# Kernel optimization log

Measured on AMD Instinct MI355X. Metric: run time of the kernel, lower is better.

The kernel has to match this reference:

```python
import jax, jax.numpy as jnp
import numpy as np

B, C, L = 1024, 256, 16   # nodes, channels (num_features), num_ell (dim of 0e+1o+2e+3o)
E = 10                    # num_elements
K3, K2, K1 = 23, 4, 1     # U-matrix path counts for correlation orders 3,2,1


def setup_inputs() -> dict:
    key = jax.random.key(0)
    ks = jax.random.split(key, 8)
    return {
        "x": jax.random.normal(ks[0], (B, C, L), jnp.float32),
        "y": jax.random.normal(ks[1], (B, E), jnp.float32),
        # U buffers (generalized Clebsch-Gordan, here random stand-ins of the right shapes)
        "U3": jax.random.normal(ks[2], (L, L, L, K3), jnp.float32),
        "U2": jax.random.normal(ks[3], (L, L, K2), jnp.float32),
        "U1": jax.random.normal(ks[4], (L, K1), jnp.float32),
        # per-element weights, scaled by 1/num_params as in the module
        "W3": jax.random.normal(ks[5], (E, K3, C), jnp.float32) / K3,
        "W2": jax.random.normal(ks[6], (E, K2, C), jnp.float32) / K2,
        "W1": jax.random.normal(ks[7], (E, K1, C), jnp.float32) / K1,
    }


def reference(x, y, U3, U2, U1, W3, W2, W1):
    # symmetric_cp, irrep_out lmax=0 (scalar output), correlation=3.
    # Main (nu=3): out[b,c,w,v] = sum_{i,k,e} U3[w,v,i,k] W3[e,k,c] x[b,c,i] y[b,e]
    # Efficient order: element-select weights, outer-product over (i,k), then one GEMM with U3.
    w3 = jnp.einsum('ekc,be->bkc', W3, y)              # [B,K3,C]
    q = jnp.einsum('bkc,bci->bcik', w3, x)             # [B,C,L,K3]
    out = jnp.einsum('wvik,bcik->bcwv', U3, q)         # [B,C,L,L]
    # nu=2: weighting then feature contraction
    w2 = jnp.einsum('ekc,be->bkc', W2, y)              # [B,K2,C]
    c2 = jnp.einsum('wvk,bkc->bcwv', U2, w2) + out     # [B,C,L,L]
    out = jnp.einsum('bcwi,bci->bcw', c2, x)           # [B,C,L]
    # nu=1
    w1 = jnp.einsum('ekc,be->bkc', W1, y)              # [B,K1,C]
    c1 = jnp.einsum('wk,bkc->bcw', U1, w1) + out       # [B,C,L]
    out = jnp.einsum('bci,bci->bc', c1, x)             # [B,C]
    return out.reshape(out.shape[0], -1)
```

## Files before the change

kernel.cpp:

```cpp
#include <hip/hip_runtime.h>


#define B_   1024
#define C_   256
#define L_   16
#define E_   10
#define K3_  23
#define K2_  4

#define NM3  816
#define NM2  136
#define MTOT 992
#define NCH2 61
#define STSTR 68

using f32x4   = __attribute__((ext_vector_type(4))) float;
using f32x16  = __attribute__((ext_vector_type(16))) float;
using short8v = __attribute__((ext_vector_type(8))) short;

__device__ __host__ __forceinline__ constexpr int tri_(int n) { return n * (n + 1) / 2; }
__device__ __host__ __forceinline__ constexpr int tet_(int n) { return n * (n + 1) * (n + 2) / 6; }

struct MTab { unsigned char a[MTOT], b[MTOT], c[MTOT]; };
constexpr MTab mkMT() {
  MTab t = {};
  int m = 0;
  for (int a = 0; a < 16; a++)
    for (int b = a; b < 16; b++)
      for (int c = b; c < 16; c++) { t.a[m] = a; t.b[m] = b; t.c[m] = c; ++m; }
  for (int a = 0; a < 16; a++)
    for (int b = a; b < 16; b++) { t.a[m] = a; t.b[m] = b; t.c[m] = 16; ++m; }
  for (int a = 0; a < 16; a++) { t.a[m] = a; t.b[m] = 16; t.c[m] = 16; ++m; }
  while (m < MTOT) { t.a[m] = 17; t.b[m] = 17; t.c[m] = 17; ++m; }
  return t;
}
constexpr MTab MT = mkMT();

__global__ void prep_kernel(const float* __restrict__ U3, const float* __restrict__ U2,
                            const float* __restrict__ U1, unsigned short* __restrict__ wsFrag) {
  __shared__ float sRow[16][36];
  const int ch = blockIdx.x;
  const int tid = threadIdx.x;
  if (tid < 16) {
    const int m = ch * 16 + tid;
    for (int i = 0; i < 36; i++) sRow[tid][i] = 0.f;
    if (m < NM3) {
      int ia = 0;
      while (tet_(16) - tet_(16 - (ia + 1)) <= m) ia++;
      int rem = m - (tet_(16) - tet_(16 - ia));
      int ib = ia;
      while (tri_(16 - ia) - tri_(16 - (ib + 1)) <= rem) ib++;
      int ic = ib + (rem - (tri_(16 - ia) - tri_(16 - ib)));
      int pw[6] = {ia, ia, ib, ib, ic, ic};
      int pv[6] = {ib, ic, ia, ic, ia, ib};
      int pi[6] = {ic, ib, ic, ia, ib, ia};
      bool use[6];
      for (int p = 0; p < 6; p++) {
        bool dup = false;
        for (int q = 0; q < p; q++)
          dup = dup || (pw[p] == pw[q] && pv[p] == pv[q] && pi[p] == pi[q]);
        use[p] = !dup;
      }
      for (int k = 0; k < K3_; k++) {
        float s = 0.f;
        for (int p = 0; p < 6; p++)
          if (use[p]) s += U3[((pw[p] * L_ + pv[p]) * L_ + pi[p]) * K3_ + k];
        sRow[tid][k] = s;
      }
    } else if (m < NM3 + NM2) {
      const int pidx = m - NM3;
      int ia = 0;
      while (136 - tri_(16 - (ia + 1)) <= pidx) ia++;
      int ib = ia + (pidx - (136 - tri_(16 - ia)));
      for (int k2 = 0; k2 < K2_; k2++) {
        float s = U2[(ia * L_ + ib) * K2_ + k2];
        if (ia != ib) s += U2[(ib * L_ + ia) * K2_ + k2];
        sRow[tid][23 + k2] = s;
      }
    } else if (m < NM3 + NM2 + L_) {
      sRow[tid][27] = U1[m - NM3 - NM2];
    }
  }
  __syncthreads();
  {
    const int lane = tid;
    unsigned short v16[8];
    for (int j = 0; j < 8; j++) {
      float v = sRow[(lane >> 5) * 8 + j][lane & 31];
      unsigned vb = __float_as_uint(v) + 0x8000u;
      v16[j] = (unsigned short)(vb >> 16);
    }
    unsigned* dst = (unsigned*)(wsFrag + ((size_t)ch * 64 + lane) * 8);
    for (int p = 0; p < 4; p++)
      dst[p] = (unsigned)v16[2 * p] | ((unsigned)v16[2 * p + 1] << 16);
  }
}

__device__ __forceinline__ void lane32_swap(unsigned& a, unsigned& b) {
#if defined(__has_builtin) && __has_builtin(__builtin_amdgcn_permlane32_swap)
  auto r = __builtin_amdgcn_permlane32_swap((int)a, (int)b, false, false);
  a = (unsigned)r[0];
  b = (unsigned)r[1];
#else
  asm volatile("v_permlane32_swap_b32 %0, %1" : "+v"(a), "+v"(b));
#endif
}

template <int M>
__device__ __forceinline__ float pval(const float (&XX)[16]) {
  if constexpr (MT.a[M] == 17) return 0.f;
  else if constexpr (MT.b[M] == 16) return XX[MT.a[M]];
  else if constexpr (MT.c[M] == 16) return XX[MT.a[M]] * XX[MT.b[M]];
  else return XX[MT.a[M]] * XX[MT.b[M]] * XX[MT.c[M]];
}

template <int CH, int I>
__device__ __forceinline__ void pk_pair(const float (&XX)[16],
                                        unsigned& o0, unsigned& o1) {
  {
    float p0 = pval<CH * 16 + 2 * I>(XX);
    float p1 = pval<CH * 16 + 2 * I + 1>(XX);
    asm("v_cvt_pk_bf16_f32 %0, %1, %2" : "=v"(o0) : "v"(p0), "v"(p1));
  }
  {
    float p0 = pval<CH * 16 + 8 + 2 * I>(XX);
    float p1 = pval<CH * 16 + 8 + 2 * I + 1>(XX);
    asm("v_cvt_pk_bf16_f32 %0, %1, %2" : "=v"(o1) : "v"(p0), "v"(p1));
  }
  lane32_swap(o0, o1);
}

template <int CH>
__device__ __forceinline__ void chunk_body(
    const float (&XX)[16], const float4* __restrict__ Bg, int lane,
    float4& nb0, float4& nb1, f32x16& acc0, f32x16& acc1) {
  unsigned pk0[4], pk1[4];
  pk_pair<CH, 0>(XX, pk0[0], pk1[0]);
  pk_pair<CH, 1>(XX, pk0[1], pk1[1]);
  pk_pair<CH, 2>(XX, pk0[2], pk1[2]);
  pk_pair<CH, 3>(XX, pk0[3], pk1[3]);

  float4 bh;
  if constexpr ((CH & 1) == 0) bh = nb0; else bh = nb1;
  if constexpr (CH + 2 < NCH2) {
    if constexpr ((CH & 1) == 0) nb0 = Bg[(CH + 2) * 64 + lane];
    else                         nb1 = Bg[(CH + 2) * 64 + lane];
  }
  short8v A0, A1, BH;
  __builtin_memcpy(&A0, pk0, 16);
  __builtin_memcpy(&A1, pk1, 16);
  __builtin_memcpy(&BH, &bh, 16);

  acc0 = __builtin_amdgcn_mfma_f32_32x32x16_bf16(A0, BH, acc0, 0, 0, 0);
  acc1 = __builtin_amdgcn_mfma_f32_32x32x16_bf16(A1, BH, acc1, 0, 0, 0);
}

template <int CH>
struct Loop {
  static __device__ __forceinline__ void run(
      const float (&XX)[16], const float4* __restrict__ Bg, int lane,
      float4& nb0, float4& nb1, f32x16& acc0, f32x16& acc1) {
    chunk_body<CH>(XX, Bg, lane, nb0, nb1, acc0, acc1);
    Loop<CH + 1>::run(XX, Bg, lane, nb0, nb1, acc0, acc1);
  }
};
template <>
struct Loop<NCH2> {
  static __device__ __forceinline__ void run(
      const float (&)[16], const float4* __restrict__, int,
      float4&, float4&, f32x16&, f32x16&) {}
};

__global__ __launch_bounds__(64, 2) void symcon_kernel(
    const float* __restrict__ x,
    const float* __restrict__ y,
    const float* __restrict__ W3,
    const float* __restrict__ W2,
    const float* __restrict__ W1,
    const unsigned short* __restrict__ wsFrag,
    float* __restrict__ out)
{
  __shared__ __attribute__((aligned(16))) float sT[28 * STSTR];

  const int lane = threadIdx.x;
  const int bb = blockIdx.x;
  const int b = bb >> 2;
  const int c = (bb & 3) * 64 + lane;

  float XX[16];
  {
    const float4* xg = (const float4*)(x + ((size_t)b * C_ + c) * L_);
    #pragma unroll
    for (int i = 0; i < 4; i++) {
      float4 v = xg[i];
      XX[i * 4 + 0] = v.x; XX[i * 4 + 1] = v.y;
      XX[i * 4 + 2] = v.z; XX[i * 4 + 3] = v.w;
    }
  }

  const float4* Bg = (const float4*)wsFrag;
  float4 nb0 = Bg[lane], nb1 = Bg[64 + lane];
  f32x16 acc0 = (f32x16)0.f, acc1 = (f32x16)0.f;

  Loop<0>::run(XX, Bg, lane, nb0, nb1, acc0, acc1);

  const int kcol = lane & 31, hi = lane >> 5;
  if (kcol < 28) {
    #pragma unroll
    for (int q = 0; q < 4; ++q) {
      f32x4 v0, v1;
      #pragma unroll
      for (int i2 = 0; i2 < 4; ++i2) {
        v0[i2] = acc0[4 * q + i2];
        v1[i2] = acc1[4 * q + i2];
      }
      *(f32x4*)&sT[kcol * STSTR +      8 * q + 4 * hi] = v0;
      *(f32x4*)&sT[kcol * STSTR + 32 + 8 * q + 4 * hi] = v1;
    }
  }
  float t[28];
  #pragma unroll
  for (int k = 0; k < 28; ++k) t[k] = sT[k * STSTR + lane];

  float yreg[E_];
  #pragma unroll
  for (int e = 0; e < E_; e++) yreg[e] = y[b * E_ + e];

  float result = 0.f;
  #pragma unroll
  for (int k = 0; k < K3_; k++) {
    const float* w3p = &W3[k * C_ + c];
    float w3k = 0.f;
    #pragma unroll
    for (int e = 0; e < E_; e++) w3k += w3p[e * K3_ * C_] * yreg[e];
    result += t[k] * w3k;
  }
  #pragma unroll
  for (int k2 = 0; k2 < K2_; k2++) {
    const float* w2p = &W2[k2 * C_ + c];
    float w2k = 0.f;
    #pragma unroll
    for (int e = 0; e < E_; e++) w2k += w2p[e * K2_ * C_] * yreg[e];
    result += t[23 + k2] * w2k;
  }
  {
    float w1v = 0.f;
    #pragma unroll
    for (int e = 0; e < E_; e++) w1v += W1[e * C_ + c] * yreg[e];
    result += t[27] * w1v;
  }

  out[(size_t)b * C_ + c] = result;
}

extern "C" void kernel_launch(void* const* d_in, const int* in_sizes, int n_in,
                              void* d_out, int out_size, void* d_ws, size_t ws_size,
                              hipStream_t stream) {
  const float* x  = (const float*)d_in[0];
  const float* y  = (const float*)d_in[1];
  const float* U3 = (const float*)d_in[2];
  const float* U2 = (const float*)d_in[3];
  const float* U1 = (const float*)d_in[4];
  const float* W3 = (const float*)d_in[5];
  const float* W2 = (const float*)d_in[6];
  const float* W1 = (const float*)d_in[7];
  float* out = (float*)d_out;

  unsigned short* wsFrag = (unsigned short*)d_ws;

  prep_kernel<<<dim3(NCH2), dim3(64), 0, stream>>>(U3, U2, U1, wsFrag);
  symcon_kernel<<<dim3(B_ * 4), dim3(64), 0, stream>>>(
      x, y, W3, W2, W1, wsFrag, out);
}
```

Measured before the change: 119.2 us.

## Split MFMA reduction chunks across two waves per block with LDS combine

Each block now runs two waves that each handle about half of the 61 K-chunks of the bf16 MFMA contraction. Wave 0 writes its partial accumulators to shared memory, and wave 1 adds them in and performs the epilogue. The goal is to halve the serial per-wave chain of packing and MFMA, exposing more waves to hide latency. The cost is an extra LDS round trip and a barrier, and wave 0 sits idle during the epilogue.

```diff
diff --git a/kernel.cpp b/kernel.cpp
--- a/kernel.cpp
+++ b/kernel.cpp
@@ -12,6 +12,7 @@
 #define NM2  136
 #define MTOT 992
 #define NCH2 61
+#define SPLIT 31
 #define STSTR 68
 
 using f32x4   = __attribute__((ext_vector_type(4))) float;
@@ -130,7 +131,7 @@
   lane32_swap(o0, o1);
 }
 
-template <int CH>
+template <int CH, int END>
 __device__ __forceinline__ void chunk_body(
     const float (&XX)[16], const float4* __restrict__ Bg, int lane,
     float4& nb0, float4& nb1, f32x16& acc0, f32x16& acc1) {
@@ -142,7 +143,7 @@
 
   float4 bh;
   if constexpr ((CH & 1) == 0) bh = nb0; else bh = nb1;
-  if constexpr (CH + 2 < NCH2) {
+  if constexpr (CH + 2 < END) {
     if constexpr ((CH & 1) == 0) nb0 = Bg[(CH + 2) * 64 + lane];
     else                         nb1 = Bg[(CH + 2) * 64 + lane];
   }
@@ -155,23 +156,23 @@
   acc1 = __builtin_amdgcn_mfma_f32_32x32x16_bf16(A1, BH, acc1, 0, 0, 0);
 }
 
-template <int CH>
-struct Loop {
+template <int CH, int END>
+struct LoopR {
   static __device__ __forceinline__ void run(
       const float (&XX)[16], const float4* __restrict__ Bg, int lane,
       float4& nb0, float4& nb1, f32x16& acc0, f32x16& acc1) {
-    chunk_body<CH>(XX, Bg, lane, nb0, nb1, acc0, acc1);
-    Loop<CH + 1>::run(XX, Bg, lane, nb0, nb1, acc0, acc1);
+    chunk_body<CH, END>(XX, Bg, lane, nb0, nb1, acc0, acc1);
+    LoopR<CH + 1, END>::run(XX, Bg, lane, nb0, nb1, acc0, acc1);
   }
 };
-template <>
-struct Loop<NCH2> {
+template <int END>
+struct LoopR<END, END> {
   static __device__ __forceinline__ void run(
       const float (&)[16], const float4* __restrict__, int,
       float4&, float4&, f32x16&, f32x16&) {}
 };
 
-__global__ __launch_bounds__(64, 2) void symcon_kernel(
+__global__ __launch_bounds__(128, 2) void symcon_kernel(
     const float* __restrict__ x,
     const float* __restrict__ y,
     const float* __restrict__ W3,
@@ -180,9 +181,11 @@
     const unsigned short* __restrict__ wsFrag,
     float* __restrict__ out)
 {
-  __shared__ __attribute__((aligned(16))) float sT[28 * STSTR];
-
-  const int lane = threadIdx.x;
+  __shared__ __attribute__((aligned(16))) float sPart[64 * 33];
+  float* sT = sPart;
+
+  const int tid = threadIdx.x;
+  const int lane = tid & 63, wid = tid >> 6;
   const int bb = blockIdx.x;
   const int b = bb >> 2;
   const int c = (bb & 3) * 64 + lane;
@@ -199,58 +202,80 @@
   }
 
   const float4* Bg = (const float4*)wsFrag;
-  float4 nb0 = Bg[lane], nb1 = Bg[64 + lane];
   f32x16 acc0 = (f32x16)0.f, acc1 = (f32x16)0.f;
-
-  Loop<0>::run(XX, Bg, lane, nb0, nb1, acc0, acc1);
-
-  const int kcol = lane & 31, hi = lane >> 5;
-  if (kcol < 28) {
-    #pragma unroll
-    for (int q = 0; q < 4; ++q) {
-      f32x4 v0, v1;
-      #pragma unroll
-      for (int i2 = 0; i2 < 4; ++i2) {
-        v0[i2] = acc0[4 * q + i2];
-        v1[i2] = acc1[4 * q + i2];
-      }
-      *(f32x4*)&sT[kcol * STSTR +      8 * q + 4 * hi] = v0;
-      *(f32x4*)&sT[kcol * STSTR + 32 + 8 * q + 4 * hi] = v1;
-    }
-  }
-  float t[28];
-  #pragma unroll
-  for (int k = 0; k < 28; ++k) t[k] = sT[k * STSTR + lane];
-
-  float yreg[E_];
-  #pragma unroll
-  for (int e = 0; e < E_; e++) yreg[e] = y[b * E_ + e];
-
-  float result = 0.f;
-  #pragma unroll
-  for (int k = 0; k < K3_; k++) {
-    const float* w3p = &W3[k * C_ + c];
-    float w3k = 0.f;
-    #pragma unroll
-    for (int e = 0; e < E_; e++) w3k += w3p[e * K3_ * C_] * yreg[e];
-    result += t[k] * w3k;
-  }
-  #pragma unroll
-  for (int k2 = 0; k2 < K2_; k2++) {
-    const float* w2p = &W2[k2 * C_ + c];
-    float w2k = 0.f;
-    #pragma unroll
-    for (int e = 0; e < E_; e++) w2k += w2p[e * K2_ * C_] * yreg[e];
-    result += t[23 + k2] * w2k;
-  }
-  {
-    float w1v = 0.f;
-    #pragma unroll
-    for (int e = 0; e < E_; e++) w1v += W1[e * C_ + c] * yreg[e];
-    result += t[27] * w1v;
-  }
-
-  out[(size_t)b * C_ + c] = result;
+  float4 nb0, nb1;
+
+  if (wid == 0) {
+    nb0 = Bg[0 * 64 + lane];
+    nb1 = Bg[1 * 64 + lane];
+    LoopR<0, SPLIT>::run(XX, Bg, lane, nb0, nb1, acc0, acc1);
+    #pragma unroll
+    for (int r = 0; r < 16; ++r) {
+      sPart[lane * 33 + r]      = acc0[r];
+      sPart[lane * 33 + 16 + r] = acc1[r];
+    }
+  } else {
+    nb1 = Bg[SPLIT * 64 + lane];
+    nb0 = Bg[(SPLIT + 1) * 64 + lane];
+    LoopR<SPLIT, NCH2>::run(XX, Bg, lane, nb0, nb1, acc0, acc1);
+  }
+  __syncthreads();
+
+  if (wid == 1) {
+    #pragma unroll
+    for (int r = 0; r < 16; ++r) {
+      acc0[r] += sPart[lane * 33 + r];
+      acc1[r] += sPart[lane * 33 + 16 + r];
+    }
+
+    const int kcol = lane & 31, hi = lane >> 5;
+    if (kcol < 28) {
+      #pragma unroll
+      for (int q = 0; q < 4; ++q) {
+        f32x4 v0, v1;
+        #pragma unroll
+        for (int i2 = 0; i2 < 4; ++i2) {
+          v0[i2] = acc0[4 * q + i2];
+          v1[i2] = acc1[4 * q + i2];
+        }
+        *(f32x4*)&sT[kcol * STSTR +      8 * q + 4 * hi] = v0;
+        *(f32x4*)&sT[kcol * STSTR + 32 + 8 * q + 4 * hi] = v1;
+      }
+    }
+    float t[28];
+    #pragma unroll
+    for (int k = 0; k < 28; ++k) t[k] = sT[k * STSTR + lane];
+
+    float yreg[E_];
+    #pragma unroll
+    for (int e = 0; e < E_; e++) yreg[e] = y[b * E_ + e];
+
+    float result = 0.f;
+    #pragma unroll
+    for (int k = 0; k < K3_; k++) {
+      const float* w3p = &W3[k * C_ + c];
+      float w3k = 0.f;
+      #pragma unroll
+      for (int e = 0; e < E_; e++) w3k += w3p[e * K3_ * C_] * yreg[e];
+      result += t[k] * w3k;
+    }
+    #pragma unroll
+    for (int k2 = 0; k2 < K2_; k2++) {
+      const float* w2p = &W2[k2 * C_ + c];
+      float w2k = 0.f;
+      #pragma unroll
+      for (int e = 0; e < E_; e++) w2k += w2p[e * K2_ * C_] * yreg[e];
+      result += t[23 + k2] * w2k;
+    }
+    {
+      float w1v = 0.f;
+      #pragma unroll
+      for (int e = 0; e < E_; e++) w1v += W1[e * C_ + c] * yreg[e];
+      result += t[27] * w1v;
+    }
+
+    out[(size_t)b * C_ + c] = result;
+  }
 }
 
 extern "C" void kernel_launch(void* const* d_in, const int* in_sizes, int n_in,
@@ -269,6 +294,6 @@
   unsigned short* wsFrag = (unsigned short*)d_ws;
 
   prep_kernel<<<dim3(NCH2), dim3(64), 0, stream>>>(U3, U2, U1, wsFrag);
-  symcon_kernel<<<dim3(B_ * 4), dim3(64), 0, stream>>>(
+  symcon_kernel<<<dim3(B_ * 4), dim3(128), 0, stream>>>(
       x, y, W3, W2, W1, wsFrag, out);
 }
```

New measurement: 122.1 us. 1.02x slower.
